# Kernel optimization log

Measured on AMD Instinct MI355X. Metric: run time of the kernel, lower is better.

## Reference

```python
import jax, jax.numpy as jnp
import numpy as np

L = 2          # num_layers
H = 1024       # hidden_size
XD = 192       # exogenous feature dim
YD = 64        # out_size == y dim
IN = XD + YD   # lstm input size
B = 256
PRE_LEN = 64
FWD_LEN = 48


def setup_inputs() -> dict:
    key = jax.random.key(0)
    ks = jax.random.split(key, 16)
    s = 0.05  # keep gate pre-activations in a sane range
    inp = {
        "pre_x": jax.random.normal(ks[0], (PRE_LEN, B, XD), jnp.float32),
        "pre_y": jax.random.normal(ks[1], (PRE_LEN, B, YD), jnp.float32),
        "forward_x": jax.random.normal(ks[2], (FWD_LEN, B, XD), jnp.float32),
        # layer 0 LSTM params (torch layout: w_ih (4H, IN), w_hh (4H, H))
        "w_ih_0": jax.random.normal(ks[3], (4 * H, IN), jnp.float32) * s,
        "w_hh_0": jax.random.normal(ks[4], (4 * H, H), jnp.float32) * s,
        "b_ih_0": jax.random.normal(ks[5], (4 * H,), jnp.float32) * s,
        "b_hh_0": jax.random.normal(ks[6], (4 * H,), jnp.float32) * s,
        # layer 1
        "w_ih_1": jax.random.normal(ks[7], (4 * H, H), jnp.float32) * s,
        "w_hh_1": jax.random.normal(ks[8], (4 * H, H), jnp.float32) * s,
        "b_ih_1": jax.random.normal(ks[9], (4 * H,), jnp.float32) * s,
        "b_hh_1": jax.random.normal(ks[10], (4 * H,), jnp.float32) * s,
        # fc: Linear(H,H) -> Tanh -> Linear(H,YD)
        "fc_w1": jax.random.normal(ks[11], (H, H), jnp.float32) * s,
        "fc_b1": jax.random.normal(ks[12], (H,), jnp.float32) * s,
        "fc_w2": jax.random.normal(ks[13], (YD, H), jnp.float32) * s,
        "fc_b2": jax.random.normal(ks[14], (YD,), jnp.float32) * s,
    }
    return inp


def _lstm_cell(x, h, c, w_ih, w_hh, b_ih, b_hh):
    # torch gate order: i, f, g, o
    z = x @ w_ih.T + h @ w_hh.T + (b_ih + b_hh)  # (B, 4H)
    i, f, g, o = jnp.split(z, 4, axis=-1)
    c_new = jax.nn.sigmoid(f) * c + jax.nn.sigmoid(i) * jnp.tanh(g)
    h_new = jax.nn.sigmoid(o) * jnp.tanh(c_new)
    return h_new, c_new


def _stack_step(layers, x_t, hs, cs):
    # layers: list of (w_ih, w_hh, b_ih, b_hh); hs, cs: (L, B, H)
    new_h, new_c = [], []
    inp = x_t
    for l, (w_ih, w_hh, b_ih, b_hh) in enumerate(layers):
        h, c = _lstm_cell(inp, hs[l], cs[l], w_ih, w_hh, b_ih, b_hh)
        new_h.append(h)
        new_c.append(c)
        inp = h
    return jnp.stack(new_h), jnp.stack(new_c), inp  # inp = top-layer output


def reference(pre_x, pre_y, forward_x,
              w_ih_0, w_hh_0, b_ih_0, b_hh_0,
              w_ih_1, w_hh_1, b_ih_1, b_hh_1,
              fc_w1, fc_b1, fc_w2, fc_b2):
    layers = [(w_ih_0, w_hh_0, b_ih_0, b_hh_0),
              (w_ih_1, w_hh_1, b_ih_1, b_hh_1)]

    def fc(x):
        return jnp.tanh(x @ fc_w1.T + fc_b1) @ fc_w2.T + fc_b2

    batch = pre_x.shape[1]
    hs0 = jnp.zeros((L, batch, H), pre_x.dtype)
    cs0 = jnp.zeros((L, batch, H), pre_x.dtype)

    # --- warmup encode over concat(pre_x, pre_y) ---
    xy = jnp.concatenate([pre_x, pre_y], axis=2)  # (PRE_LEN, B, IN)

    def enc_step(carry, x_t):
        hs, cs = carry
        hs, cs, top = _stack_step(layers, x_t, hs, cs)
        return (hs, cs), top

    (hs, cs), enc_outs = jax.lax.scan(enc_step, (hs0, cs0), xy)
    top = enc_outs[-1]          # output[-1] from the encoding pass
    last_y = pre_y[-1]

    def dec_step(carry, fx_t):
        hs, cs, top, last_y = carry
        est = fc(top) + last_y                        # (B, YD)
        x_in = jnp.concatenate([fx_t, est], axis=1)   # (B, IN)
        hs, cs, top = _stack_step(layers, x_in, hs, cs)
        return (hs, cs, top, est), est

    _, est_all = jax.lax.scan(dec_step, (hs, cs, top, last_y), forward_x)
    return est_all  # (FWD_LEN, B, YD)
```

## Files before the change

### kernel.cpp

```cpp
#include <hip/hip_runtime.h>
#include <stdint.h>

typedef unsigned short u16;
typedef unsigned long long u64;
typedef __attribute__((ext_vector_type(8))) _Float16 f16x8;
typedef __attribute__((ext_vector_type(4))) float f32x4;

#define AGT __HIP_MEMORY_SCOPE_AGENT

__device__ inline f16x8 ldfrag(const u16* p) { return *(const f16x8*)p; }
__device__ inline u64 ldq_dev(const void* p) {
    return __hip_atomic_load((const u64*)p, __ATOMIC_RELAXED, AGT);
}
__device__ inline void stq_dev(void* p, u64 v) {
    __hip_atomic_store((u64*)p, v, __ATOMIC_RELAXED, AGT);
}
__device__ inline f16x8 ldfrag_dev(const u16* p) {
    union { u64 q[2]; f16x8 v; } u;
    u.q[0] = ldq_dev(p);
    u.q[1] = ldq_dev(p + 4);
    return u.v;
}
__device__ inline u16 f2h(float x) {
    _Float16 h = (_Float16)x;
    union { _Float16 h; u16 u; } v; v.h = h;
    return v.u;
}
__device__ inline float sigmoidf_(float x) { return 1.0f / (1.0f + expf(-x)); }

__device__ inline void gbar(unsigned* bars, int ph) {
    __syncthreads();
    if (threadIdx.x == 0) {
        __hip_atomic_fetch_add(&bars[ph], 1u, __ATOMIC_RELAXED, AGT);
        while (__hip_atomic_load(&bars[ph], __ATOMIC_RELAXED, AGT) < 256u)
            __builtin_amdgcn_s_sleep(2);
    }
    __syncthreads();
}


typedef f32x4 RedT[8][64];

__device__ __forceinline__ void lstm_unit(
    const u16* __restrict__ AFa, int KBa,
    const u16* __restrict__ BFa,
    const u16* __restrict__ AFh,
    const u16* __restrict__ BFh,
    const float* __restrict__ bsum,
    float* __restrict__ c,
    u16* __restrict__ h_out,
    int ct, int mg, int tid, RedT* red, u16* stage)
{
    const int w    = tid >> 6;
    const int lane = tid & 63;
    const int l15  = lane & 15;
    const int quad = lane >> 4;

    f32x4 acc[4][4];
    #pragma unroll
    for (int t = 0; t < 4; ++t)
        #pragma unroll
        for (int g = 0; g < 4; ++g) acc[t][g] = (f32x4){0, 0, 0, 0};

    {
        const int q = KBa >> 2;
        #pragma unroll 2
        for (int kb = w * q; kb < w * q + q; ++kb) {
            f16x8 a[4], b[4];
            #pragma unroll
            for (int t = 0; t < 4; ++t)
                a[t] = ldfrag_dev(AFa + (((size_t)(mg * 4 + t) * KBa + kb) * 64 + lane) * 8);
            #pragma unroll
            for (int g = 0; g < 4; ++g)
                b[g] = ldfrag(BFa + (((size_t)(ct * 4 + g) * KBa + kb) * 64 + lane) * 8);
            #pragma unroll
            for (int t = 0; t < 4; ++t)
                #pragma unroll
                for (int g = 0; g < 4; ++g)
                    acc[t][g] = __builtin_amdgcn_mfma_f32_16x16x32_f16(a[t], b[g], acc[t][g], 0, 0, 0);
        }
    }
    {
        #pragma unroll 2
        for (int kb = w * 8; kb < w * 8 + 8; ++kb) {
            f16x8 a[4], b[4];
            #pragma unroll
            for (int t = 0; t < 4; ++t)
                a[t] = ldfrag_dev(AFh + (((size_t)(mg * 4 + t) * 32 + kb) * 64 + lane) * 8);
            #pragma unroll
            for (int g = 0; g < 4; ++g)
                b[g] = ldfrag(BFh + (((size_t)(ct * 4 + g) * 32 + kb) * 64 + lane) * 8);
            #pragma unroll
            for (int t = 0; t < 4; ++t)
                #pragma unroll
                for (int g = 0; g < 4; ++g)
                    acc[t][g] = __builtin_amdgcn_mfma_f32_16x16x32_f16(a[t], b[g], acc[t][g], 0, 0, 0);
        }
    }

    f32x4 z[4];
    #pragma unroll
    for (int t = 0; t < 2; ++t)
        #pragma unroll
        for (int g = 0; g < 4; ++g)
            red[w][t * 4 + g][lane] = acc[t][g];
    __syncthreads();
    if (w < 2)
        #pragma unroll
        for (int g = 0; g < 4; ++g)
            z[g] = red[0][w * 4 + g][lane] + red[1][w * 4 + g][lane] +
                   red[2][w * 4 + g][lane] + red[3][w * 4 + g][lane];
    __syncthreads();
    #pragma unroll
    for (int t = 0; t < 2; ++t)
        #pragma unroll
        for (int g = 0; g < 4; ++g)
            red[w][t * 4 + g][lane] = acc[t + 2][g];
    __syncthreads();
    if (w >= 2)
        #pragma unroll
        for (int g = 0; g < 4; ++g)
            z[g] = red[0][(w - 2) * 4 + g][lane] + red[1][(w - 2) * 4 + g][lane] +
                   red[2][(w - 2) * 4 + g][lane] + red[3][(w - 2) * 4 + g][lane];

    const int col = ct * 16 + l15;
    float bv[4];
    #pragma unroll
    for (int g = 0; g < 4; ++g) bv[g] = bsum[g * 1024 + col];
    const int mtile = mg * 4 + w;
    #pragma unroll
    for (int r = 0; r < 4; ++r) {
        const int rl  = quad * 4 + r;
        const int row = mtile * 16 + rl;
        const size_t gi = (size_t)row * 1024 + col;
        const float zi = z[0][r] + bv[0];
        const float zf = z[1][r] + bv[1];
        const float zg = z[2][r] + bv[2];
        const float zo = z[3][r] + bv[3];
        const float cv = c[gi];
        const float cn = sigmoidf_(zf) * cv + sigmoidf_(zi) * tanhf(zg);
        c[gi] = cn;
        stage[(w * 16 + rl) * 16 + l15] = f2h(sigmoidf_(zo) * tanhf(cn));
    }
    __syncthreads();
    {
        const int half  = tid & 1;
        const int chunk = tid >> 1;
        const int qh    = chunk & 1;
        const int rb    = chunk >> 1;
        const int mt    = mg * 4 + (rb >> 4), rl = rb & 15;
        const int hkb   = ct >> 1, hq = (ct & 1) * 2 + qh;
        u64 v = *(const u64*)&stage[rb * 16 + qh * 8 + half * 4];
        stq_dev(h_out + (((size_t)mt * 32 + hkb) * 64 + hq * 16 + rl) * 8 + half * 4, v);
    }
}

__device__ __forceinline__ void fc1_unit(
    const u16* __restrict__ AFx, const u16* __restrict__ BFw,
    const float* __restrict__ bias, u16* __restrict__ U,
    int ctq, int mg, int tid, RedT* red, u16* stage)
{
    const int w    = tid >> 6;
    const int lane = tid & 63;
    const int l15  = lane & 15;
    const int quad = lane >> 4;

    f32x4 acc[4][4];
    #pragma unroll
    for (int t = 0; t < 4; ++t)
        #pragma unroll
        for (int g = 0; g < 4; ++g) acc[t][g] = (f32x4){0, 0, 0, 0};

    #pragma unroll 2
    for (int kb = w * 8; kb < w * 8 + 8; ++kb) {
        f16x8 a[4], b[4];
        #pragma unroll
        for (int t = 0; t < 4; ++t)
            a[t] = ldfrag_dev(AFx + (((size_t)(mg * 4 + t) * 32 + kb) * 64 + lane) * 8);
        #pragma unroll
        for (int g = 0; g < 4; ++g)
            b[g] = ldfrag(BFw + (((size_t)(ctq * 4 + g) * 32 + kb) * 64 + lane) * 8);
        #pragma unroll
        for (int t = 0; t < 4; ++t)
            #pragma unroll
            for (int g = 0; g < 4; ++g)
                acc[t][g] = __builtin_amdgcn_mfma_f32_16x16x32_f16(a[t], b[g], acc[t][g], 0, 0, 0);
    }

    f32x4 z[4];
    #pragma unroll
    for (int t = 0; t < 2; ++t)
        #pragma unroll
        for (int g = 0; g < 4; ++g)
            red[w][t * 4 + g][lane] = acc[t][g];
    __syncthreads();
    if (w < 2)
        #pragma unroll
        for (int g = 0; g < 4; ++g)
            z[g] = red[0][w * 4 + g][lane] + red[1][w * 4 + g][lane] +
                   red[2][w * 4 + g][lane] + red[3][w * 4 + g][lane];
    __syncthreads();
    #pragma unroll
    for (int t = 0; t < 2; ++t)
        #pragma unroll
        for (int g = 0; g < 4; ++g)
            red[w][t * 4 + g][lane] = acc[t + 2][g];
    __syncthreads();
    if (w >= 2)
        #pragma unroll
        for (int g = 0; g < 4; ++g)
            z[g] = red[0][(w - 2) * 4 + g][lane] + red[1][(w - 2) * 4 + g][lane] +
                   red[2][(w - 2) * 4 + g][lane] + red[3][(w - 2) * 4 + g][lane];

    #pragma unroll
    for (int g = 0; g < 4; ++g) {
        const float bv = bias[ctq * 64 + g * 16 + l15];
        #pragma unroll
        for (int r = 0; r < 4; ++r)
            stage[(w * 16 + quad * 4 + r) * 64 + g * 16 + l15] = f2h(tanhf(z[g][r] + bv));
    }
    __syncthreads();
    #pragma unroll
    for (int s = 0; s < 4; ++s) {
        const int i    = s * 256 + tid;
        const int half = i & 1;
        const int cg   = (i >> 1) & 7;
        const int rb   = i >> 4;
        const int col0 = ctq * 64 + cg * 8;
        const int ukb  = col0 >> 5, uq = (col0 >> 3) & 3;
        const int mt   = mg * 4 + (rb >> 4), rl = rb & 15;
        u64 v = *(const u64*)&stage[rb * 64 + cg * 8 + half * 4];
        stq_dev(U + (((size_t)mt * 32 + ukb) * 64 + uq * 16 + rl) * 8 + half * 4, v);
    }
}

__device__ __forceinline__ void fc2_unit(
    const u16* __restrict__ AFu, const u16* __restrict__ BFw2,
    const float* __restrict__ b2,
    const float* __restrict__ est_in, float* __restrict__ est_out,
    float* __restrict__ out_t, u16* __restrict__ xdec_t,
    int mtile, int tid, u16* stage)
{
    const int w    = tid >> 6;
    const int lane = tid & 63;
    const int l15  = lane & 15;
    const int quad = lane >> 4;

    f32x4 accp[4] = {{0,0,0,0},{0,0,0,0},{0,0,0,0},{0,0,0,0}};
    const u16* ap = AFu + ((size_t)(mtile * 32) * 64 + lane) * 8;
    const u16* bp = BFw2 + ((size_t)(w * 32) * 64 + lane) * 8;
    #pragma unroll 4
    for (int kb = 0; kb < 32; ++kb)
        accp[kb & 3] = __builtin_amdgcn_mfma_f32_16x16x32_f16(
            ldfrag_dev(ap + kb * 512), ldfrag(bp + kb * 512), accp[kb & 3], 0, 0, 0);
    f32x4 acc = accp[0] + accp[1] + accp[2] + accp[3];

    const int col = w * 16 + l15;
    const float bv = b2[col];
    #pragma unroll
    for (int r = 0; r < 4; ++r) {
        const int rl = quad * 4 + r;
        const int row = mtile * 16 + rl;
        const float v = acc[r] + bv + est_in[row * 64 + col];
        est_out[row * 64 + col] = v;
        out_t[row * 64 + col] = v;
        stage[rl * 64 + col] = f2h(v);
    }
    __syncthreads();
    {
        const int half = tid & 1;
        const int cg   = (tid >> 1) & 7;
        const int rr   = tid >> 4;
        const int col0 = 192 + cg * 8;
        const int xkb  = col0 >> 5, xq = (col0 >> 3) & 3;
        u64 v = *(const u64*)&stage[rr * 64 + cg * 8 + half * 4];
        stq_dev(xdec_t + (((size_t)mtile * 8 + xkb) * 64 + xq * 16 + rr) * 8 + half * 4, v);
    }
}

struct MegaP {
    const u16 *xyenc; u16 *xdec;
    const u16 *wih0, *whh0, *wih1, *whh1, *fcw1, *fcw2;
    const float *b0s, *b1s, *fcb1, *fcb2;
    float *c0, *c1, *est0, *est1, *out;
    u16 *h0a, *h0b, *h1a, *h1b, *U;
    unsigned *bars;
};

__global__ __launch_bounds__(256, 1) void mega_k(MegaP p) {
    __shared__ f32x4 red[4][8][64];
    __shared__ u16 stage[4096];
    const int b   = blockIdx.x;
    const int tid = threadIdx.x;
    const int ct  = b & 63;
    const int mg  = b >> 6;

    u16* h0buf[2] = { p.h0a, p.h0b };
    u16* h1buf[2] = { p.h1a, p.h1b };
    float* estb[2] = { p.est0, p.est1 };
    int ph = 0;

    for (int s = 0; s <= 64; ++s) {
        if (s < 64)
            lstm_unit(p.xyenc + (size_t)s * 65536, 8, p.wih0,
                      h0buf[s & 1], p.whh0, p.b0s, p.c0, h0buf[(s + 1) & 1],
                      ct, mg, tid, red, stage);
        if (s >= 1) {
            const int t = s - 1;
            lstm_unit(h0buf[(t + 1) & 1], 32, p.wih1,
                      h1buf[t & 1], p.whh1, p.b1s, p.c1, h1buf[(t + 1) & 1],
                      ct, mg, tid, red, stage);
        }
        gbar(p.bars, ph++);
    }

    int cur = 0;
    for (int t = 0; t < 48; ++t) {
        if (b < 64)
            fc1_unit(h1buf[cur], p.fcw1, p.fcb1, p.U, b & 15, b >> 4, tid, red, stage);
        gbar(p.bars, ph++);
        if (b < 16)
            fc2_unit(p.U, p.fcw2, p.fcb2, estb[t & 1], estb[(t + 1) & 1],
                     p.out + (size_t)t * 16384, p.xdec + (size_t)t * 65536, b, tid, stage);
        gbar(p.bars, ph++);
        lstm_unit(p.xdec + (size_t)t * 65536, 8, p.wih0,
                  h0buf[cur], p.whh0, p.b0s, p.c0, h0buf[cur ^ 1],
                  ct, mg, tid, red, stage);
        gbar(p.bars, ph++);
        lstm_unit(h0buf[cur ^ 1], 32, p.wih1,
                  h1buf[cur], p.whh1, p.b1s, p.c1, h1buf[cur ^ 1],
                  ct, mg, tid, red, stage);
        gbar(p.bars, ph++);
        cur ^= 1;
    }
}

__global__ __launch_bounds__(256, 2) void enc_phase_k(MegaP p, int ph) {
    __shared__ f32x4 red[4][8][64];
    __shared__ u16 stage[4096];
    const int b   = blockIdx.x;
    const int tid = threadIdx.x;
    u16* h0buf[2] = { p.h0a, p.h0b };
    u16* h1buf[2] = { p.h1a, p.h1b };
    if (b < 256) {
        if (ph < 64)
            lstm_unit(p.xyenc + (size_t)ph * 65536, 8, p.wih0,
                      h0buf[ph & 1], p.whh0, p.b0s, p.c0, h0buf[(ph + 1) & 1],
                      b & 63, b >> 6, tid, red, stage);
    } else {
        if (ph >= 1) {
            const int t = ph - 1, bb = b - 256;
            lstm_unit(h0buf[(t + 1) & 1], 32, p.wih1,
                      h1buf[t & 1], p.whh1, p.b1s, p.c1, h1buf[(t + 1) & 1],
                      bb & 63, bb >> 6, tid, red, stage);
        }
    }
}
__global__ __launch_bounds__(256, 2) void fc1_fb_k(MegaP p, int cur) {
    __shared__ f32x4 red[4][8][64];
    __shared__ u16 stage[4096];
    u16* h1buf[2] = { p.h1a, p.h1b };
    fc1_unit(h1buf[cur], p.fcw1, p.fcb1, p.U,
             blockIdx.x & 15, blockIdx.x >> 4, threadIdx.x, red, stage);
}
__global__ __launch_bounds__(256, 2) void fc2_fb_k(MegaP p, int t) {
    __shared__ u16 stage[4096];
    float* estb[2] = { p.est0, p.est1 };
    fc2_unit(p.U, p.fcw2, p.fcb2, estb[t & 1], estb[(t + 1) & 1],
             p.out + (size_t)t * 16384, p.xdec + (size_t)t * 65536,
             blockIdx.x, threadIdx.x, stage);
}
__global__ __launch_bounds__(256, 2) void l0_fb_k(MegaP p, int t, int cur) {
    __shared__ f32x4 red[4][8][64];
    __shared__ u16 stage[4096];
    u16* h0buf[2] = { p.h0a, p.h0b };
    lstm_unit(p.xdec + (size_t)t * 65536, 8, p.wih0,
              h0buf[cur], p.whh0, p.b0s, p.c0, h0buf[cur ^ 1],
              blockIdx.x & 63, blockIdx.x >> 6, threadIdx.x, red, stage);
}
__global__ __launch_bounds__(256, 2) void l1_fb_k(MegaP p, int cur) {
    __shared__ f32x4 red[4][8][64];
    __shared__ u16 stage[4096];
    u16* h0buf[2] = { p.h0a, p.h0b };
    u16* h1buf[2] = { p.h1a, p.h1b };
    lstm_unit(h0buf[cur ^ 1], 32, p.wih1,
              h1buf[cur], p.whh1, p.b1s, p.c1, h1buf[cur ^ 1],
              blockIdx.x & 63, blockIdx.x >> 6, threadIdx.x, red, stage);
}

__global__ void cvt_bfrag_k(const float* __restrict__ src, u16* __restrict__ dst,
                            int K, int kbshift, int S1, int S2, int total) {
    int i = blockIdx.x * 256 + threadIdx.x;
    if (i >= total) return;
    const int lane = i & 63;
    const int kb   = (i >> 6) & ((1 << kbshift) - 1);
    const int rest = i >> (6 + kbshift);
    const int sub  = rest & 3;
    const int grp  = rest >> 2;
    const int row  = sub * S1 + grp * S2 + (lane & 15);
    const int colK = kb * 32 + (lane >> 4) * 8;
    const float* s = src + (size_t)row * K + colK;
    u16* d = dst + (size_t)i * 8;
    #pragma unroll
    for (int j = 0; j < 8; ++j) d[j] = f2h(s[j]);
}
__global__ void bias_k(const float* __restrict__ a, const float* __restrict__ b,
                       float* __restrict__ d, int n) {
    int i = blockIdx.x * 256 + threadIdx.x;
    if (i < n) d[i] = a[i] + b[i];
}
__global__ void init_k(u16* h0, u16* h1, float* c0, float* c1) {
    int i = blockIdx.x * 256 + threadIdx.x;
    h0[i] = 0; h1[i] = 0; c0[i] = 0.0f; c1[i] = 0.0f;
}
__global__ void estinit_k(const float* __restrict__ pre_y, float* __restrict__ est_prev) {
    int i = blockIdx.x * 256 + threadIdx.x;
    est_prev[i] = pre_y[63 * 16384 + i];
}
__global__ void pack_enc_k(const float* __restrict__ pre_x, const float* __restrict__ pre_y,
                           u16* __restrict__ xy) {
    int i = blockIdx.x * 256 + threadIdx.x;
    const int lane  = i & 63;
    const int kb    = (i >> 6) & 7;
    const int mtile = (i >> 9) & 15;
    const int t     = i >> 13;
    const int row   = mtile * 16 + (lane & 15);
    const int cb    = kb * 32 + (lane >> 4) * 8;
    u16* d = xy + (size_t)i * 8;
    #pragma unroll
    for (int j = 0; j < 8; ++j) {
        const int col = cb + j;
        const float v = (col < 192) ? pre_x[((size_t)t * 256 + row) * 192 + col]
                                    : pre_y[((size_t)t * 256 + row) * 64 + (col - 192)];
        d[j] = f2h(v);
    }
}
__global__ void pack_dec_k(const float* __restrict__ fx, u16* __restrict__ xd,
                           int total_threads) {
    int i = blockIdx.x * 256 + threadIdx.x;
    if (i >= total_threads) return;
    const int lane  = i & 63;
    int rest = i >> 6;
    const int kb    = rest % 6;  rest /= 6;
    const int mtile = rest & 15;
    const int t     = rest >> 4;
    const int row   = mtile * 16 + (lane & 15);
    const int cb    = kb * 32 + (lane >> 4) * 8;
    u16* d = xd + ((((size_t)t * 16 + mtile) * 8 + kb) * 64 + lane) * 8;
    #pragma unroll
    for (int j = 0; j < 8; ++j)
        d[j] = f2h(fx[((size_t)t * 256 + row) * 192 + cb + j]);
}

extern "C" void kernel_launch(void* const* d_in, const int* in_sizes, int n_in,
                              void* d_out, int out_size, void* d_ws, size_t ws_size,
                              hipStream_t stream) {
    const float* pre_x  = (const float*)d_in[0];
    const float* pre_y  = (const float*)d_in[1];
    const float* fx     = (const float*)d_in[2];
    const float* w_ih_0 = (const float*)d_in[3];
    const float* w_hh_0 = (const float*)d_in[4];
    const float* b_ih_0 = (const float*)d_in[5];
    const float* b_hh_0 = (const float*)d_in[6];
    const float* w_ih_1 = (const float*)d_in[7];
    const float* w_hh_1 = (const float*)d_in[8];
    const float* b_ih_1 = (const float*)d_in[9];
    const float* b_hh_1 = (const float*)d_in[10];
    const float* fc_w1  = (const float*)d_in[11];
    const float* fc_b1  = (const float*)d_in[12];
    const float* fc_w2  = (const float*)d_in[13];
    const float* fc_b2  = (const float*)d_in[14];

    size_t off = 0;
    char* wsb = (char*)d_ws;
    auto alloc = [&](size_t bytes) -> void* {
        void* p = wsb + off;
        off += (bytes + 255) & ~(size_t)255;
        return p;
    };
    u16* wih0 = (u16*)alloc((size_t)4096 * 256 * 2);
    u16* whh0 = (u16*)alloc((size_t)4096 * 1024 * 2);
    u16* wih1 = (u16*)alloc((size_t)4096 * 1024 * 2);
    u16* whh1 = (u16*)alloc((size_t)4096 * 1024 * 2);
    u16* fcw1 = (u16*)alloc((size_t)1024 * 1024 * 2);
    u16* fcw2 = (u16*)alloc((size_t)64 * 1024 * 2);
    float* b0s = (float*)alloc(4096 * 4);
    float* b1s = (float*)alloc(4096 * 4);
    u16* xyenc = (u16*)alloc((size_t)64 * 256 * 256 * 2);
    u16* xdec  = (u16*)alloc((size_t)48 * 256 * 256 * 2);
    u16* h0a = (u16*)alloc((size_t)256 * 1024 * 2);
    u16* h0b = (u16*)alloc((size_t)256 * 1024 * 2);
    u16* h1a = (u16*)alloc((size_t)256 * 1024 * 2);
    u16* h1b = (u16*)alloc((size_t)256 * 1024 * 2);
    float* c0 = (float*)alloc((size_t)256 * 1024 * 4);
    float* c1 = (float*)alloc((size_t)256 * 1024 * 4);
    u16* ufc  = (u16*)alloc((size_t)256 * 1024 * 2);
    float* est0 = (float*)alloc((size_t)256 * 64 * 4);
    float* est1 = (float*)alloc((size_t)256 * 64 * 4);
    unsigned* bars = (unsigned*)alloc(4096);

    hipMemsetAsync(bars, 0, 4096, stream);
    cvt_bfrag_k<<<512, 256, 0, stream>>>(w_ih_0, wih0, 256, 3, 1024, 16, 64 * 4 * 8 * 64);
    cvt_bfrag_k<<<2048, 256, 0, stream>>>(w_hh_0, whh0, 1024, 5, 1024, 16, 64 * 4 * 32 * 64);
    cvt_bfrag_k<<<2048, 256, 0, stream>>>(w_ih_1, wih1, 1024, 5, 1024, 16, 64 * 4 * 32 * 64);
    cvt_bfrag_k<<<2048, 256, 0, stream>>>(w_hh_1, whh1, 1024, 5, 1024, 16, 64 * 4 * 32 * 64);
    cvt_bfrag_k<<<512, 256, 0, stream>>>(fc_w1, fcw1, 1024, 5, 16, 64, 16 * 4 * 32 * 64);
    cvt_bfrag_k<<<32, 256, 0, stream>>>(fc_w2, fcw2, 1024, 5, 16, 0, 1 * 4 * 32 * 64);
    bias_k<<<16, 256, 0, stream>>>(b_ih_0, b_hh_0, b0s, 4096);
    bias_k<<<16, 256, 0, stream>>>(b_ih_1, b_hh_1, b1s, 4096);
    init_k<<<1024, 256, 0, stream>>>(h0a, h1a, c0, c1);
    estinit_k<<<64, 256, 0, stream>>>(pre_y, est0);
    pack_enc_k<<<2048, 256, 0, stream>>>(pre_x, pre_y, xyenc);
    pack_dec_k<<<1152, 256, 0, stream>>>(fx, xdec, 48 * 16 * 6 * 64);

    MegaP prm;
    prm.xyenc = xyenc;  prm.xdec = xdec;
    prm.wih0 = wih0;  prm.whh0 = whh0;  prm.wih1 = wih1;  prm.whh1 = whh1;
    prm.fcw1 = fcw1;  prm.fcw2 = fcw2;
    prm.b0s = b0s;  prm.b1s = b1s;  prm.fcb1 = fc_b1;  prm.fcb2 = fc_b2;
    prm.c0 = c0;  prm.c1 = c1;  prm.est0 = est0;  prm.est1 = est1;
    prm.out = (float*)d_out;
    prm.h0a = h0a;  prm.h0b = h0b;  prm.h1a = h1a;  prm.h1b = h1b;  prm.U = ufc;
    prm.bars = bars;

    void* kargs[] = { (void*)&prm };
    hipError_t ce = hipLaunchCooperativeKernel((const void*)mega_k, dim3(256), dim3(256),
                                               kargs, 0, stream);
    if (ce != hipSuccess) {
        for (int ph = 0; ph <= 64; ++ph)
            enc_phase_k<<<512, 256, 0, stream>>>(prm, ph);
        int cur = 0;
        for (int t = 0; t < 48; ++t) {
            fc1_fb_k<<<64, 256, 0, stream>>>(prm, cur);
            fc2_fb_k<<<16, 256, 0, stream>>>(prm, t);
            l0_fb_k<<<256, 256, 0, stream>>>(prm, t, cur);
            l1_fb_k<<<256, 256, 0, stream>>>(prm, cur);
            cur ^= 1;
        }
    }
}
```

Before: 4.328 ms.

## Stage activation fragments through double-buffered LDS with prefetch in GEMM loops

Replaces the per-wave direct global loads of activation (A) fragments with a cooperative, double-buffered LDS staging scheme. All 256 threads load the next chunk of 4 k-blocks while the current chunk is consumed by MFMAs, and the k-split across waves becomes interleaved per chunk. The reduction and stage buffers now alias the same shared memory as the A buffer. This aims to hide device-scope load latency by prefetching, at the cost of a block barrier on every chunk iteration.

```diff
diff --git a/kernel.cpp b/kernel.cpp
--- a/kernel.cpp
+++ b/kernel.cpp
@@ -39,7 +39,60 @@
 }
 
 
-typedef f32x4 RedT[8][64];
+__device__ __forceinline__ void stage_load(const u16* AF, int KBT, int mg, int c,
+                                           int tid, f16x8 v[4]) {
+    #pragma unroll
+    for (int i = 0; i < 4; ++i) {
+        const int f   = i * 256 + tid;
+        const int mtL = f >> 8;
+        const int kbL = (f >> 6) & 3;
+        const int ln  = f & 63;
+        v[i] = ldfrag_dev(AF + (((size_t)(mg * 4 + mtL) * KBT + c * 4 + kbL) * 64 + ln) * 8);
+    }
+}
+__device__ __forceinline__ void stage_write(u16* buf, int tid, const f16x8 v[4]) {
+    #pragma unroll
+    for (int i = 0; i < 4; ++i)
+        *(f16x8*)(buf + (size_t)(i * 256 + tid) * 8) = v[i];
+}
+
+__device__ __forceinline__ void gemm_side(
+    const u16* AF, int KBT, const u16* BF, int nt0,
+    int mg, int tid, u16* Abuf, f32x4 acc[4][4])
+{
+    const int w    = tid >> 6;
+    const int lane = tid & 63;
+    const int NC   = KBT >> 2;
+
+    f16x8 pre[4];
+    stage_load(AF, KBT, mg, 0, tid, pre);
+    stage_write(Abuf, tid, pre);
+    __syncthreads();
+
+    for (int c = 0; c < NC; ++c) {
+        const bool more = (c + 1 < NC);
+        f16x8 nxt[4];
+        if (more) stage_load(AF, KBT, mg, c + 1, tid, nxt);
+
+        const u16* ab = Abuf + (c & 1) * 8192;
+        const int kb = c * 4 + w;
+        f16x8 a[4], b[4];
+        #pragma unroll
+        for (int t = 0; t < 4; ++t)
+            a[t] = *(const f16x8*)(ab + ((t * 4 + w) * 64 + lane) * 8);
+        #pragma unroll
+        for (int g = 0; g < 4; ++g)
+            b[g] = ldfrag(BF + (((size_t)(nt0 + g) * KBT + kb) * 64 + lane) * 8);
+        #pragma unroll
+        for (int t = 0; t < 4; ++t)
+            #pragma unroll
+            for (int g = 0; g < 4; ++g)
+                acc[t][g] = __builtin_amdgcn_mfma_f32_16x16x32_f16(a[t], b[g], acc[t][g], 0, 0, 0);
+
+        if (more) stage_write(Abuf + ((c + 1) & 1) * 8192, tid, nxt);
+        __syncthreads();
+    }
+}
 
 __device__ __forceinline__ void lstm_unit(
     const u16* __restrict__ AFa, int KBa,
@@ -47,10 +100,14 @@
     const u16* __restrict__ AFh,
     const u16* __restrict__ BFh,
     const float* __restrict__ bsum,
-    float* __restrict__ c,
+    float* __restrict__ cst,
     u16* __restrict__ h_out,
-    int ct, int mg, int tid, RedT* red, u16* stage)
+    int ct, int mg, int tid, char* smem)
 {
+    u16* Abuf  = (u16*)smem;
+    f32x4 (*red)[8][64] = (f32x4 (*)[8][64])smem;
+    u16* stage = (u16*)(smem + 32768);
+
     const int w    = tid >> 6;
     const int lane = tid & 63;
     const int l15  = lane & 15;
@@ -62,41 +119,8 @@
         #pragma unroll
         for (int g = 0; g < 4; ++g) acc[t][g] = (f32x4){0, 0, 0, 0};
 
-    {
-        const int q = KBa >> 2;
-        #pragma unroll 2
-        for (int kb = w * q; kb < w * q + q; ++kb) {
-            f16x8 a[4], b[4];
-            #pragma unroll
-            for (int t = 0; t < 4; ++t)
-                a[t] = ldfrag_dev(AFa + (((size_t)(mg * 4 + t) * KBa + kb) * 64 + lane) * 8);
-            #pragma unroll
-            for (int g = 0; g < 4; ++g)
-                b[g] = ldfrag(BFa + (((size_t)(ct * 4 + g) * KBa + kb) * 64 + lane) * 8);
-            #pragma unroll
-            for (int t = 0; t < 4; ++t)
-                #pragma unroll
-                for (int g = 0; g < 4; ++g)
-                    acc[t][g] = __builtin_amdgcn_mfma_f32_16x16x32_f16(a[t], b[g], acc[t][g], 0, 0, 0);
-        }
-    }
-    {
-        #pragma unroll 2
-        for (int kb = w * 8; kb < w * 8 + 8; ++kb) {
-            f16x8 a[4], b[4];
-            #pragma unroll
-            for (int t = 0; t < 4; ++t)
-                a[t] = ldfrag_dev(AFh + (((size_t)(mg * 4 + t) * 32 + kb) * 64 + lane) * 8);
-            #pragma unroll
-            for (int g = 0; g < 4; ++g)
-                b[g] = ldfrag(BFh + (((size_t)(ct * 4 + g) * 32 + kb) * 64 + lane) * 8);
-            #pragma unroll
-            for (int t = 0; t < 4; ++t)
-                #pragma unroll
-                for (int g = 0; g < 4; ++g)
-                    acc[t][g] = __builtin_amdgcn_mfma_f32_16x16x32_f16(a[t], b[g], acc[t][g], 0, 0, 0);
-        }
-    }
+    gemm_side(AFa, KBa, BFa, ct * 4, mg, tid, Abuf, acc);
+    gemm_side(AFh, 32,  BFh, ct * 4, mg, tid, Abuf, acc);
 
     f32x4 z[4];
     #pragma unroll
@@ -137,9 +161,9 @@
         const float zf = z[1][r] + bv[1];
         const float zg = z[2][r] + bv[2];
         const float zo = z[3][r] + bv[3];
-        const float cv = c[gi];
+        const float cv = cst[gi];
         const float cn = sigmoidf_(zf) * cv + sigmoidf_(zi) * tanhf(zg);
-        c[gi] = cn;
+        cst[gi] = cn;
         stage[(w * 16 + rl) * 16 + l15] = f2h(sigmoidf_(zo) * tanhf(cn));
     }
     __syncthreads();
@@ -158,8 +182,12 @@
 __device__ __forceinline__ void fc1_unit(
     const u16* __restrict__ AFx, const u16* __restrict__ BFw,
     const float* __restrict__ bias, u16* __restrict__ U,
-    int ctq, int mg, int tid, RedT* red, u16* stage)
+    int ctq, int mg, int tid, char* smem)
 {
+    u16* Abuf  = (u16*)smem;
+    f32x4 (*red)[8][64] = (f32x4 (*)[8][64])smem;
+    u16* stage = (u16*)(smem + 32768);
+
     const int w    = tid >> 6;
     const int lane = tid & 63;
     const int l15  = lane & 15;
@@ -171,21 +199,7 @@
         #pragma unroll
         for (int g = 0; g < 4; ++g) acc[t][g] = (f32x4){0, 0, 0, 0};
 
-    #pragma unroll 2
-    for (int kb = w * 8; kb < w * 8 + 8; ++kb) {
-        f16x8 a[4], b[4];
-        #pragma unroll
-        for (int t = 0; t < 4; ++t)
-            a[t] = ldfrag_dev(AFx + (((size_t)(mg * 4 + t) * 32 + kb) * 64 + lane) * 8);
-        #pragma unroll
-        for (int g = 0; g < 4; ++g)
-            b[g] = ldfrag(BFw + (((size_t)(ctq * 4 + g) * 32 + kb) * 64 + lane) * 8);
-        #pragma unroll
-        for (int t = 0; t < 4; ++t)
-            #pragma unroll
-            for (int g = 0; g < 4; ++g)
-                acc[t][g] = __builtin_amdgcn_mfma_f32_16x16x32_f16(a[t], b[g], acc[t][g], 0, 0, 0);
-    }
+    gemm_side(AFx, 32, BFw, ctq * 4, mg, tid, Abuf, acc);
 
     f32x4 z[4];
     #pragma unroll
@@ -239,8 +253,9 @@
     const float* __restrict__ b2,
     const float* __restrict__ est_in, float* __restrict__ est_out,
     float* __restrict__ out_t, u16* __restrict__ xdec_t,
-    int mtile, int tid, u16* stage)
+    int mtile, int tid, char* smem)
 {
+    u16* stage = (u16*)(smem + 32768);
     const int w    = tid >> 6;
     const int lane = tid & 63;
     const int l15  = lane & 15;
@@ -288,8 +303,7 @@
 };
 
 __global__ __launch_bounds__(256, 1) void mega_k(MegaP p) {
-    __shared__ f32x4 red[4][8][64];
-    __shared__ u16 stage[4096];
+    __shared__ char smem[40960];
     const int b   = blockIdx.x;
     const int tid = threadIdx.x;
     const int ct  = b & 63;
@@ -304,12 +318,12 @@
         if (s < 64)
             lstm_unit(p.xyenc + (size_t)s * 65536, 8, p.wih0,
                       h0buf[s & 1], p.whh0, p.b0s, p.c0, h0buf[(s + 1) & 1],
-                      ct, mg, tid, red, stage);
+                      ct, mg, tid, smem);
         if (s >= 1) {
             const int t = s - 1;
             lstm_unit(h0buf[(t + 1) & 1], 32, p.wih1,
                       h1buf[t & 1], p.whh1, p.b1s, p.c1, h1buf[(t + 1) & 1],
-                      ct, mg, tid, red, stage);
+                      ct, mg, tid, smem);
         }
         gbar(p.bars, ph++);
     }
@@ -317,27 +331,26 @@
     int cur = 0;
     for (int t = 0; t < 48; ++t) {
         if (b < 64)
-            fc1_unit(h1buf[cur], p.fcw1, p.fcb1, p.U, b & 15, b >> 4, tid, red, stage);
+            fc1_unit(h1buf[cur], p.fcw1, p.fcb1, p.U, b & 15, b >> 4, tid, smem);
         gbar(p.bars, ph++);
         if (b < 16)
             fc2_unit(p.U, p.fcw2, p.fcb2, estb[t & 1], estb[(t + 1) & 1],
-                     p.out + (size_t)t * 16384, p.xdec + (size_t)t * 65536, b, tid, stage);
+                     p.out + (size_t)t * 16384, p.xdec + (size_t)t * 65536, b, tid, smem);
         gbar(p.bars, ph++);
         lstm_unit(p.xdec + (size_t)t * 65536, 8, p.wih0,
                   h0buf[cur], p.whh0, p.b0s, p.c0, h0buf[cur ^ 1],
-                  ct, mg, tid, red, stage);
+                  ct, mg, tid, smem);
         gbar(p.bars, ph++);
         lstm_unit(h0buf[cur ^ 1], 32, p.wih1,
                   h1buf[cur], p.whh1, p.b1s, p.c1, h1buf[cur ^ 1],
-                  ct, mg, tid, red, stage);
+                  ct, mg, tid, smem);
         gbar(p.bars, ph++);
         cur ^= 1;
     }
 }
 
 __global__ __launch_bounds__(256, 2) void enc_phase_k(MegaP p, int ph) {
-    __shared__ f32x4 red[4][8][64];
-    __shared__ u16 stage[4096];
+    __shared__ char smem[40960];
     const int b   = blockIdx.x;
     const int tid = threadIdx.x;
     u16* h0buf[2] = { p.h0a, p.h0b };
@@ -346,46 +359,43 @@
         if (ph < 64)
             lstm_unit(p.xyenc + (size_t)ph * 65536, 8, p.wih0,
                       h0buf[ph & 1], p.whh0, p.b0s, p.c0, h0buf[(ph + 1) & 1],
-                      b & 63, b >> 6, tid, red, stage);
+                      b & 63, b >> 6, tid, smem);
     } else {
         if (ph >= 1) {
             const int t = ph - 1, bb = b - 256;
             lstm_unit(h0buf[(t + 1) & 1], 32, p.wih1,
                       h1buf[t & 1], p.whh1, p.b1s, p.c1, h1buf[(t + 1) & 1],
-                      bb & 63, bb >> 6, tid, red, stage);
+                      bb & 63, bb >> 6, tid, smem);
         }
     }
 }
 __global__ __launch_bounds__(256, 2) void fc1_fb_k(MegaP p, int cur) {
-    __shared__ f32x4 red[4][8][64];
-    __shared__ u16 stage[4096];
+    __shared__ char smem[40960];
     u16* h1buf[2] = { p.h1a, p.h1b };
     fc1_unit(h1buf[cur], p.fcw1, p.fcb1, p.U,
-             blockIdx.x & 15, blockIdx.x >> 4, threadIdx.x, red, stage);
+             blockIdx.x & 15, blockIdx.x >> 4, threadIdx.x, smem);
 }
 __global__ __launch_bounds__(256, 2) void fc2_fb_k(MegaP p, int t) {
-    __shared__ u16 stage[4096];
+    __shared__ char smem[40960];
     float* estb[2] = { p.est0, p.est1 };
     fc2_unit(p.U, p.fcw2, p.fcb2, estb[t & 1], estb[(t + 1) & 1],
              p.out + (size_t)t * 16384, p.xdec + (size_t)t * 65536,
-             blockIdx.x, threadIdx.x, stage);
+             blockIdx.x, threadIdx.x, smem);
 }
 __global__ __launch_bounds__(256, 2) void l0_fb_k(MegaP p, int t, int cur) {
-    __shared__ f32x4 red[4][8][64];
-    __shared__ u16 stage[4096];
+    __shared__ char smem[40960];
     u16* h0buf[2] = { p.h0a, p.h0b };
     lstm_unit(p.xdec + (size_t)t * 65536, 8, p.wih0,
               h0buf[cur], p.whh0, p.b0s, p.c0, h0buf[cur ^ 1],
-              blockIdx.x & 63, blockIdx.x >> 6, threadIdx.x, red, stage);
+              blockIdx.x & 63, blockIdx.x >> 6, threadIdx.x, smem);
 }
 __global__ __launch_bounds__(256, 2) void l1_fb_k(MegaP p, int cur) {
-    __shared__ f32x4 red[4][8][64];
-    __shared__ u16 stage[4096];
+    __shared__ char smem[40960];
     u16* h0buf[2] = { p.h0a, p.h0b };
     u16* h1buf[2] = { p.h1a, p.h1b };
     lstm_unit(h0buf[cur ^ 1], 32, p.wih1,
               h1buf[cur], p.whh1, p.b1s, p.c1, h1buf[cur ^ 1],
-              blockIdx.x & 63, blockIdx.x >> 6, threadIdx.x, red, stage);
+              blockIdx.x & 63, blockIdx.x >> 6, threadIdx.x, smem);
 }
 
 __global__ void cvt_bfrag_k(const float* __restrict__ src, u16* __restrict__ dst,
```

Result: slower. 5.963 ms (+37.8%).
